# Performance work log

Hardware: AMD Instinct MI355X
Metric: run time of the kernel (lower is better)

## Reference

```python
import math
import jax, jax.numpy as jnp
import numpy as np

D_MODEL = 128
NUM_HEADS = 8
FACTOR = 5


def setup_inputs() -> dict:
    key = jax.random.key(0)
    ks = jax.random.split(key, 9)
    B, L, dm = 2, 4096, D_MODEL
    s = 1.0 / math.sqrt(dm)
    return {
        "x": jax.random.normal(ks[0], (B, L, dm), dtype=jnp.float32),
        "Wq": jax.random.normal(ks[1], (dm, dm), dtype=jnp.float32) * s,
        "bq": jnp.zeros((dm,), jnp.float32),
        "Wk": jax.random.normal(ks[2], (dm, dm), dtype=jnp.float32) * s,
        "bk": jnp.zeros((dm,), jnp.float32),
        "Wv": jax.random.normal(ks[3], (dm, dm), dtype=jnp.float32) * s,
        "bv": jnp.zeros((dm,), jnp.float32),
        "Wo": jax.random.normal(ks[4], (dm, dm), dtype=jnp.float32) * s,
        "bo": jnp.zeros((dm,), jnp.float32),
    }


def reference(x, Wq, bq, Wk, bk, Wv, bv, Wo, bo):
    B, L, dm = x.shape
    H = NUM_HEADS
    D = dm // H
    inv_sqrt_d = 1.0 / math.sqrt(D)

    def split_heads(t):  # [B,L,dm] -> [B,H,L,D]
        return t.reshape(B, L, H, D).transpose(0, 2, 1, 3)

    Q = split_heads(x @ Wq + bq)
    K = split_heads(x @ Wk + bk)
    V = split_heads(x @ Wv + bv)

    # sample_k = min(L_K, int(log(L_K) * factor)); L is static under jit
    sample_k = min(L, int(math.log(L) * FACTOR))

    # _prob_QK: full scores, per-query stable exp, mean over queries, top-k keys
    scores_full = jnp.einsum("bhqd,bhkd->bhqk", Q, K) * inv_sqrt_d  # [B,H,L,L]
    m = jnp.max(scores_full, axis=-1, keepdims=True)
    e = jnp.exp(scores_full - m)
    mean_attn = jnp.mean(e, axis=2)  # [B,H,L_K]
    _, idx = jax.lax.top_k(mean_attn, sample_k)  # [B,H,sample_k]

    # gather sampled keys/values along the key axis
    Ks = jnp.take_along_axis(K, idx[..., None], axis=2)  # [B,H,s,D]
    Vs = jnp.take_along_axis(V, idx[..., None], axis=2)

    attn = jax.nn.softmax(jnp.einsum("bhqd,bhsd->bhqs", Q, Ks) * inv_sqrt_d, axis=-1)
    out = jnp.einsum("bhqs,bhsd->bhqd", attn, Vs)  # [B,H,L,D]
    out = out.transpose(0, 2, 1, 3).reshape(B, L, dm)
    return out @ Wo + bo
```

## Files before the change

kernel.cpp:

```cpp
#include <hip/hip_runtime.h>
#include <hip/hip_bf16.h>

#define L 4096
#define DM 128
#define NH 8
#define HD 16
#define NBH 16
#define SK 41
#define NSPLIT 8
#define SLICE (L/NSPLIT)
#define NST (SLICE/32)
#define QSCALE 0.36067376022224085f

typedef __attribute__((ext_vector_type(8))) short s16x8;
typedef __attribute__((ext_vector_type(4))) float f32x4;
typedef __attribute__((ext_vector_type(16))) float f32x16;

__device__ __forceinline__ float bf2f(unsigned short h){ return __uint_as_float(((unsigned)h)<<16); }
__device__ __forceinline__ unsigned short f2bf(float f){
  unsigned u = __float_as_uint(f);
  u += 0x7FFFu + ((u>>16)&1u);
  return (unsigned short)(u>>16);
}
__device__ __forceinline__ float fast_exp2(float x){
  float r;
  asm("v_exp_f32 %0, %1" : "=v"(r) : "v"(x));
  return r;
}

__global__ __launch_bounds__(256) void prep(
    const float* __restrict__ x,
    const float* __restrict__ Wq, const float* __restrict__ Wk,
    const float* __restrict__ Wv, const float* __restrict__ Wo,
    unsigned short* __restrict__ Xh, unsigned short* __restrict__ Xl,
    unsigned short* __restrict__ Wph, unsigned short* __restrict__ Wpl)
{
  const int t = threadIdx.x;
  const int blk = blockIdx.x;
  if (blk < 1024){
    const long base = (long)blk*1024 + t*4;
    float4 v = *(const float4*)(x + base);
    unsigned short h[4], lo[4];
    h[0]=f2bf(v.x); lo[0]=f2bf(v.x - bf2f(h[0]));
    h[1]=f2bf(v.y); lo[1]=f2bf(v.y - bf2f(h[1]));
    h[2]=f2bf(v.z); lo[2]=f2bf(v.z - bf2f(h[2]));
    h[3]=f2bf(v.w); lo[3]=f2bf(v.w - bf2f(h[3]));
    *(uint2*)(Xh+base) = *(uint2*)h;
    *(uint2*)(Xl+base) = *(uint2*)lo;
  } else {
    const int e = (blk-1024)*256 + t;
    const int p = e >> 14;
    const int idx = e & 16383;
    const int j = idx & 7;
    const int f = idx >> 3;
    const int n = f & 127;
    const int kcg = f >> 7;
    const int k = (kcg>>1)*16 + (kcg&1)*8 + j;
    const float* W = (p==0)?Wq:((p==1)?Wk:((p==2)?Wv:Wo));
    const float v = W[k*128 + n];
    const unsigned short h = f2bf(v);
    Wph[e] = h;
    Wpl[e] = f2bf(v - bf2f(h));
  }
}

__global__ __launch_bounds__(256) void proj_mfma(
    const unsigned short* __restrict__ Xh, const unsigned short* __restrict__ Xl,
    const unsigned short* __restrict__ Wph, const unsigned short* __restrict__ Wpl,
    const float* __restrict__ bq, const float* __restrict__ bk, const float* __restrict__ bv,
    unsigned short* __restrict__ Qh, unsigned short* __restrict__ Ql,
    unsigned short* __restrict__ Kh, unsigned short* __restrict__ Kl,
    float* __restrict__ Vo)
{
  const int p = blockIdx.y;
  const float* __restrict__ bias = (p==0)?bq:((p==1)?bk:bv);
  __shared__ __align__(16) unsigned short wh[16384];
  __shared__ __align__(16) unsigned short wl[16384];
  const int t = threadIdx.x;
  {
    const uint4* gh = (const uint4*)(Wph + (long)p*16384);
    const uint4* gl = (const uint4*)(Wpl + (long)p*16384);
    uint4* sh = (uint4*)wh; uint4* sl = (uint4*)wl;
#pragma unroll
    for (int i=0;i<8;++i){ sh[t + i*256] = gh[t + i*256]; sl[t + i*256] = gl[t + i*256]; }
  }
  __syncthreads();
  const int w = t>>6, l = t&63;
  const int lc = l&15, g = l>>4;
  const int mbase = blockIdx.x*128 + w*32;
  f32x4 acc[2][8];
#pragma unroll
  for (int mt=0;mt<2;++mt)
#pragma unroll
    for (int nt=0;nt<8;++nt){ acc[mt][nt][0]=0.f; acc[mt][nt][1]=0.f; acc[mt][nt][2]=0.f; acc[mt][nt][3]=0.f; }
  const unsigned short* __restrict__ Asrc = (g<2)? Xh : Xl;
  const int koff = (g&1)*8;
  for (int kc=0; kc<8; ++kc){
    s16x8 a[2];
#pragma unroll
    for (int mt=0;mt<2;++mt)
      a[mt] = *(const s16x8*)(Asrc + ((long)(mbase + mt*16 + lc))*128 + kc*16 + koff);
#pragma unroll
    for (int nt=0;nt<8;++nt){
      const int fi = (kc*2+(g&1))*128 + nt*16 + lc;
      s16x8 b1 = ((const s16x8*)wh)[fi];
      s16x8 b2 = ((const s16x8*)wl)[fi];
#pragma unroll
      for (int mt=0;mt<2;++mt){
        acc[mt][nt] = __builtin_amdgcn_mfma_f32_16x16x32_bf16(a[mt], b1, acc[mt][nt], 0,0,0);
        acc[mt][nt] = __builtin_amdgcn_mfma_f32_16x16x32_bf16(a[mt], b2, acc[mt][nt], 0,0,0);
      }
    }
  }
#pragma unroll
  for (int nt=0;nt<8;++nt){
    const float bb = bias[nt*16 + lc];
#pragma unroll
    for (int mt=0;mt<2;++mt){
#pragma unroll
      for (int r=0;r<4;++r){
        const int row = mbase + mt*16 + g*4 + r;
        float v = acc[mt][nt][r] + bb;
        const int b = row>>12, li = row&4095;
        const long o = (((long)(b*NH + nt))*L + li)*HD + lc;
        if (p==2){
          Vo[o] = v;
        } else {
          if (p==0) v *= QSCALE;
          const unsigned short h = f2bf(v);
          const unsigned short lo2 = f2bf(v - bf2f(h));
          if (p==0){ Qh[o]=h; Ql[o]=lo2; } else { Kh[o]=h; Kl[o]=lo2; }
        }
      }
    }
  }
}

__global__ __launch_bounds__(256) void rowmax_k(
    const unsigned short* __restrict__ Qh, const unsigned short* __restrict__ Ql,
    const unsigned short* __restrict__ Kh, const unsigned short* __restrict__ Kl,
    float* __restrict__ mpart)
{
  const int bh = blockIdx.y, qt = blockIdx.x, ks = blockIdx.z;
  const int t = threadIdx.x, w = t>>6, l = t&63;
  const int lk = l&31, ks8 = (l>>5)*8;
  const int qbase = qt*256 + w*64;
  s16x8 ah0, al0, ah1, al1;
  {
    const long r0 = ((long)bh*L + qbase + lk)*HD + ks8;
    ah0 = *(const s16x8*)(Qh + r0);
    al0 = *(const s16x8*)(Ql + r0);
    ah1 = *(const s16x8*)(Qh + r0 + 32*HD);
    al1 = *(const s16x8*)(Ql + r0 + 32*HD);
  }
  f32x16 fz, rmax0, rmax1;
#pragma unroll
  for (int r=0;r<16;++r){ fz[r]=0.f; rmax0[r]=-3.4e38f; rmax1[r]=-3.4e38f; }
  const unsigned short* khp = Kh + ((long)bh*L + ks*SLICE + lk)*HD + ks8;
  const unsigned short* klp = Kl + ((long)bh*L + ks*SLICE + lk)*HD + ks8;
#pragma unroll 2
  for (int st=0; st<NST; ++st){
    s16x8 bhi = *(const s16x8*)(khp + st*32*HD);
    s16x8 blo = *(const s16x8*)(klp + st*32*HD);
    f32x16 a0 = __builtin_amdgcn_mfma_f32_32x32x16_bf16(ah0, bhi, fz, 0,0,0);
    a0 = __builtin_amdgcn_mfma_f32_32x32x16_bf16(al0, bhi, a0, 0,0,0);
    a0 = __builtin_amdgcn_mfma_f32_32x32x16_bf16(ah0, blo, a0, 0,0,0);
    f32x16 a1 = __builtin_amdgcn_mfma_f32_32x32x16_bf16(ah1, bhi, fz, 0,0,0);
    a1 = __builtin_amdgcn_mfma_f32_32x32x16_bf16(al1, bhi, a1, 0,0,0);
    a1 = __builtin_amdgcn_mfma_f32_32x32x16_bf16(ah1, blo, a1, 0,0,0);
#pragma unroll
    for (int r=0;r<16;++r){
      rmax0[r] = fmaxf(rmax0[r], a0[r]);
      rmax1[r] = fmaxf(rmax1[r], a1[r]);
    }
  }
  const long obase = ((long)ks*NBH + bh)*L + qbase + 4*(l>>5);
#pragma unroll
  for (int r=0;r<16;++r){
    float v0 = rmax0[r], v1 = rmax1[r];
    v0 = fmaxf(v0, __shfl_xor(v0,1));  v1 = fmaxf(v1, __shfl_xor(v1,1));
    v0 = fmaxf(v0, __shfl_xor(v0,2));  v1 = fmaxf(v1, __shfl_xor(v1,2));
    v0 = fmaxf(v0, __shfl_xor(v0,4));  v1 = fmaxf(v1, __shfl_xor(v1,4));
    v0 = fmaxf(v0, __shfl_xor(v0,8));  v1 = fmaxf(v1, __shfl_xor(v1,8));
    v0 = fmaxf(v0, __shfl_xor(v0,16)); v1 = fmaxf(v1, __shfl_xor(v1,16));
    if (lk == 0){
      const int rmap = (r&3) + 8*(r>>2);
      mpart[obase + rmap]      = v0;
      mpart[obase + 32 + rmap] = v1;
    }
  }
}

__global__ __launch_bounds__(256) void mreduce(
    const float* __restrict__ mpart, float* __restrict__ wq)
{
  const int i = blockIdx.x*256 + threadIdx.x;
  float m = -3.4e38f;
#pragma unroll
  for (int p=0;p<NSPLIT;++p) m = fmaxf(m, mpart[(long)p*NBH*L + i]);
  wq[i] = fast_exp2(-m);
}

__global__ __launch_bounds__(256) void colexp_k(
    const unsigned short* __restrict__ Kh, const unsigned short* __restrict__ Kl,
    const unsigned short* __restrict__ Qh, const unsigned short* __restrict__ Ql,
    const float* __restrict__ wq, float* __restrict__ cspart)
{
  const int bh = blockIdx.y, kt = blockIdx.x, qs = blockIdx.z;
  const int t = threadIdx.x, w = t>>6, l = t&63;
  const int lk = l&31, ks8 = (l>>5)*8;
  const int kbase = kt*256 + w*64;
  s16x8 ah0, al0, ah1, al1;
  {
    const long r0 = ((long)bh*L + kbase + lk)*HD + ks8;
    ah0 = *(const s16x8*)(Kh + r0);
    al0 = *(const s16x8*)(Kl + r0);
    ah1 = *(const s16x8*)(Kh + r0 + 32*HD);
    al1 = *(const s16x8*)(Kl + r0 + 32*HD);
  }
  f32x16 fz, cs0, cs1;
#pragma unroll
  for (int r=0;r<16;++r){ fz[r]=0.f; cs0[r]=0.f; cs1[r]=0.f; }
  const unsigned short* qhp = Qh + ((long)bh*L + qs*SLICE + lk)*HD + ks8;
  const unsigned short* qlp = Ql + ((long)bh*L + qs*SLICE + lk)*HD + ks8;
  const float* wgp = wq + (long)bh*L + qs*SLICE + lk;
#pragma unroll 2
  for (int st=0; st<NST; ++st){
    s16x8 bhi = *(const s16x8*)(qhp + st*32*HD);
    s16x8 blo = *(const s16x8*)(qlp + st*32*HD);
    const float wv = wgp[st*32];
    f32x16 a0 = __builtin_amdgcn_mfma_f32_32x32x16_bf16(ah0, bhi, fz, 0,0,0);
    a0 = __builtin_amdgcn_mfma_f32_32x32x16_bf16(al0, bhi, a0, 0,0,0);
    a0 = __builtin_amdgcn_mfma_f32_32x32x16_bf16(ah0, blo, a0, 0,0,0);
    f32x16 a1 = __builtin_amdgcn_mfma_f32_32x32x16_bf16(ah1, bhi, fz, 0,0,0);
    a1 = __builtin_amdgcn_mfma_f32_32x32x16_bf16(al1, bhi, a1, 0,0,0);
    a1 = __builtin_amdgcn_mfma_f32_32x32x16_bf16(ah1, blo, a1, 0,0,0);
#pragma unroll
    for (int r=0;r<16;++r){
      cs0[r] = fmaf(fast_exp2(a0[r]), wv, cs0[r]);
      cs1[r] = fmaf(fast_exp2(a1[r]), wv, cs1[r]);
    }
  }
  const long obase = ((long)qs*NBH + bh)*L + kbase + 4*(l>>5);
#pragma unroll
  for (int r=0;r<16;++r){
    float v0 = cs0[r], v1 = cs1[r];
    v0 += __shfl_xor(v0,1);  v1 += __shfl_xor(v1,1);
    v0 += __shfl_xor(v0,2);  v1 += __shfl_xor(v1,2);
    v0 += __shfl_xor(v0,4);  v1 += __shfl_xor(v1,4);
    v0 += __shfl_xor(v0,8);  v1 += __shfl_xor(v1,8);
    v0 += __shfl_xor(v0,16); v1 += __shfl_xor(v1,16);
    if (lk == 0){
      const int rmap = (r&3) + 8*(r>>2);
      cspart[obase + rmap]      = v0;
      cspart[obase + 32 + rmap] = v1;
    }
  }
}

__global__ __launch_bounds__(256) void topk_gather(
    const float* __restrict__ cspart,
    const unsigned short* __restrict__ Kh, const unsigned short* __restrict__ Kl,
    const float* __restrict__ V,
    float* __restrict__ Ks, float* __restrict__ Vs)
{
  const int bh = blockIdx.x;
  const int t = threadIdx.x;
  __shared__ float vals[4096];
  __shared__ unsigned hist[2048];
  __shared__ unsigned suf[256];
  __shared__ int meta[4];
  __shared__ int sel[SK];
  __shared__ int sorted[SK];
  __shared__ int tiei[4096];

  for (int i=t; i<1024; i+=256){
    float4 s = {0.f,0.f,0.f,0.f};
#pragma unroll
    for (int p=0;p<NSPLIT;++p){
      float4 v = *(const float4*)(cspart + ((long)p*NBH + bh)*L + i*4);
      s.x += v.x; s.y += v.y; s.z += v.z; s.w += v.w;
    }
    *(float4*)&vals[i*4] = s;
  }
  __syncthreads();

  int target = SK;
  unsigned B1 = 0, P2 = 0, T = 0;
#pragma unroll
  for (int pass=0; pass<3; ++pass){
    const int nb = (pass<2) ? 2048 : 1024;
    const int chunk = nb >> 8;
    for (int i=t;i<nb;i+=256) hist[i]=0u;
    __syncthreads();
    for (int i=t;i<4096;i+=256){
      const unsigned u = __float_as_uint(vals[i]);
      bool ok; int bk;
      if (pass==0){ ok = true;              bk = (int)(u>>21); }
      else if (pass==1){ ok = ((u>>21)==B1); bk = (int)((u>>10)&0x7FFu); }
      else { ok = ((u>>10)==P2);            bk = (int)(u&0x3FFu); }
      if (ok) atomicAdd(&hist[bk], 1u);
    }
    __syncthreads();
    {
      unsigned c=0;
#pragma unroll
      for (int b=0;b<8;++b) if (b<chunk) c += hist[t*chunk+b];
      suf[t]=c;
    }
    __syncthreads();
    for (int off=1; off<256; off<<=1){
      unsigned add = (t+off<256)? suf[t+off] : 0u;
      __syncthreads();
      suf[t] += add;
      __syncthreads();
    }
    {
      const unsigned mysuf = suf[t];
      const unsigned nxt = (t==255)?0u:suf[t+1];
      if (mysuf >= (unsigned)target && nxt < (unsigned)target){
        unsigned running = nxt;
        for (int b=t*chunk+chunk-1; b>=t*chunk; --b){
          const unsigned h = hist[b];
          if (running + h >= (unsigned)target){ meta[0]=b; meta[1]=(int)running; break; }
          running += h;
        }
      }
    }
    __syncthreads();
    const unsigned B = (unsigned)meta[0];
    target -= meta[1];
    if (pass==0) B1 = B;
    else if (pass==1) P2 = (B1<<11)|B;
    else T = (P2<<10)|B;
    __syncthreads();
  }
  if (t==0){ meta[2]=0; meta[3]=0; }
  __syncthreads();
  for (int i=t;i<4096;i+=256){
    const unsigned u = __float_as_uint(vals[i]);
    if (u > T){ int p = atomicAdd(&meta[2],1); sel[p]=i; }
    else if (u == T){ int p = atomicAdd(&meta[3],1); tiei[p]=i; }
  }
  __syncthreads();
  const int ngt = meta[2];
  const int ntie = meta[3];
  for (int j=t; j<ntie; j+=256){
    const int x = tiei[j];
    int rk=0;
    for (int k=0;k<ntie;++k) rk += (tiei[k] < x);
    if (rk < target) sel[ngt+rk] = x;
  }
  __syncthreads();
  if (t<SK){
    int x=sel[t]; int rk=0;
    for (int j=0;j<SK;++j) rk += (sel[j]<x);
    sorted[rk]=x;
  }
  __syncthreads();
  for (int i=t;i<SK*HD;i+=256){
    const int j=i>>4, dd=i&15;
    const int key=sorted[j];
    const long src=((long)bh*L+key)*HD+dd;
    Ks[(long)bh*SK*HD+i]=bf2f(Kh[src])+bf2f(Kl[src]);
    Vs[(long)bh*SK*HD+i]=V[src];
  }
}

__global__ __launch_bounds__(256) void sattn(
    const unsigned short* __restrict__ Qh, const unsigned short* __restrict__ Ql,
    const float* __restrict__ Ks, const float* __restrict__ Vs,
    unsigned short* __restrict__ AOh, unsigned short* __restrict__ AOl)
{
  const int bh = blockIdx.y, qb = blockIdx.x;
  const int t = threadIdx.x;
  __shared__ float ks[SK*HD], vs[SK*HD];
  for (int i=t; i<SK*HD; i+=256){
    ks[i] = Ks[(long)bh*SK*HD + i];
    vs[i] = Vs[(long)bh*SK*HD + i];
  }
  __syncthreads();
  const int q = qb*128 + (t>>1);
  const int half = t&1;
  const long qo = ((long)bh*L + q)*HD;
  float qv[16];
  {
    s16x8 h0 = *(const s16x8*)(Qh+qo);
    s16x8 h1 = *(const s16x8*)(Qh+qo+8);
    s16x8 l0 = *(const s16x8*)(Ql+qo);
    s16x8 l1 = *(const s16x8*)(Ql+qo+8);
#pragma unroll
    for (int d=0; d<8; ++d){
      qv[d]   = bf2f((unsigned short)h0[d]) + bf2f((unsigned short)l0[d]);
      qv[d+8] = bf2f((unsigned short)h1[d]) + bf2f((unsigned short)l1[d]);
    }
  }
  float mrun = -3.4e38f, lrun = 0.f, out[16];
#pragma unroll
  for (int d=0; d<16; ++d) out[d] = 0.f;
  for (int j=half; j<SK; j+=2){
    float4 k0 = *(const float4*)&ks[j*HD+0];
    float4 k1 = *(const float4*)&ks[j*HD+4];
    float4 k2 = *(const float4*)&ks[j*HD+8];
    float4 k3 = *(const float4*)&ks[j*HD+12];
    float s = qv[0]*k0.x;
    s = fmaf(qv[1],k0.y,s); s = fmaf(qv[2],k0.z,s); s = fmaf(qv[3],k0.w,s);
    s = fmaf(qv[4],k1.x,s); s = fmaf(qv[5],k1.y,s); s = fmaf(qv[6],k1.z,s); s = fmaf(qv[7],k1.w,s);
    s = fmaf(qv[8],k2.x,s); s = fmaf(qv[9],k2.y,s); s = fmaf(qv[10],k2.z,s); s = fmaf(qv[11],k2.w,s);
    s = fmaf(qv[12],k3.x,s); s = fmaf(qv[13],k3.y,s); s = fmaf(qv[14],k3.z,s); s = fmaf(qv[15],k3.w,s);
    if (s > mrun){
      const float c = fast_exp2(mrun - s);
      lrun *= c;
#pragma unroll
      for (int d=0; d<16; ++d) out[d] *= c;
      mrun = s;
    }
    const float p = fast_exp2(s - mrun);
    lrun += p;
    float4 v0 = *(const float4*)&vs[j*HD+0];
    float4 v1 = *(const float4*)&vs[j*HD+4];
    float4 v2 = *(const float4*)&vs[j*HD+8];
    float4 v3 = *(const float4*)&vs[j*HD+12];
    out[0]=fmaf(p,v0.x,out[0]); out[1]=fmaf(p,v0.y,out[1]); out[2]=fmaf(p,v0.z,out[2]); out[3]=fmaf(p,v0.w,out[3]);
    out[4]=fmaf(p,v1.x,out[4]); out[5]=fmaf(p,v1.y,out[5]); out[6]=fmaf(p,v1.z,out[6]); out[7]=fmaf(p,v1.w,out[7]);
    out[8]=fmaf(p,v2.x,out[8]); out[9]=fmaf(p,v2.y,out[9]); out[10]=fmaf(p,v2.z,out[10]); out[11]=fmaf(p,v2.w,out[11]);
    out[12]=fmaf(p,v3.x,out[12]); out[13]=fmaf(p,v3.y,out[13]); out[14]=fmaf(p,v3.z,out[14]); out[15]=fmaf(p,v3.w,out[15]);
  }
  const float mo = __shfl_xor(mrun, 1);
  const float lo = __shfl_xor(lrun, 1);
  const float mm = fmaxf(mrun, mo);
  const float cs_ = fast_exp2(mrun - mm);
  const float co_ = fast_exp2(mo - mm);
  const float ltot = fmaf(lrun, cs_, lo*co_);
  const float inv = 1.f / ltot;
#pragma unroll
  for (int d=0; d<16; ++d){
    const float ov = __shfl_xor(out[d], 1);
    out[d] = fmaf(out[d]*cs_, inv, ov*co_*inv);
  }
  if (half == 0){
    const int b = bh>>3, h = bh&7;
    const long row = (long)b*L + q;
    unsigned short hv[16], lv[16];
#pragma unroll
    for (int d=0; d<16; ++d){
      const float v = out[d];
      hv[d] = f2bf(v);
      lv[d] = f2bf(v - bf2f(hv[d]));
    }
    unsigned short* oh = AOh + row*DM + h*HD;
    unsigned short* ol = AOl + row*DM + h*HD;
    *(uint4*)(oh)   = *(uint4*)(hv);
    *(uint4*)(oh+8) = *(uint4*)(hv+8);
    *(uint4*)(ol)   = *(uint4*)(lv);
    *(uint4*)(ol+8) = *(uint4*)(lv+8);
  }
}

__global__ __launch_bounds__(256) void outproj_mfma(
    const unsigned short* __restrict__ AOh, const unsigned short* __restrict__ AOl,
    const unsigned short* __restrict__ Wph, const unsigned short* __restrict__ Wpl,
    const float* __restrict__ bo, float* __restrict__ out)
{
  __shared__ __align__(16) unsigned short wh[16384];
  __shared__ __align__(16) unsigned short wl[16384];
  const int t = threadIdx.x;
  {
    const uint4* gh = (const uint4*)(Wph + (long)3*16384);
    const uint4* gl = (const uint4*)(Wpl + (long)3*16384);
    uint4* sh = (uint4*)wh; uint4* sl = (uint4*)wl;
#pragma unroll
    for (int i=0;i<8;++i){ sh[t + i*256] = gh[t + i*256]; sl[t + i*256] = gl[t + i*256]; }
  }
  __syncthreads();
  const int w = t>>6, l = t&63;
  const int lc = l&15, g = l>>4;
  const int mbase = blockIdx.x*128 + w*32;
  f32x4 acc[2][8];
#pragma unroll
  for (int mt=0;mt<2;++mt)
#pragma unroll
    for (int nt=0;nt<8;++nt){ acc[mt][nt][0]=0.f; acc[mt][nt][1]=0.f; acc[mt][nt][2]=0.f; acc[mt][nt][3]=0.f; }
  const unsigned short* __restrict__ Asrc = (g<2)? AOh : AOl;
  const int koff = (g&1)*8;
  for (int kc=0; kc<8; ++kc){
    s16x8 a[2];
#pragma unroll
    for (int mt=0;mt<2;++mt)
      a[mt] = *(const s16x8*)(Asrc + ((long)(mbase + mt*16 + lc))*128 + kc*16 + koff);
#pragma unroll
    for (int nt=0;nt<8;++nt){
      const int fi = (kc*2+(g&1))*128 + nt*16 + lc;
      s16x8 b1 = ((const s16x8*)wh)[fi];
      s16x8 b2 = ((const s16x8*)wl)[fi];
#pragma unroll
      for (int mt=0;mt<2;++mt){
        acc[mt][nt] = __builtin_amdgcn_mfma_f32_16x16x32_bf16(a[mt], b1, acc[mt][nt], 0,0,0);
        acc[mt][nt] = __builtin_amdgcn_mfma_f32_16x16x32_bf16(a[mt], b2, acc[mt][nt], 0,0,0);
      }
    }
  }
#pragma unroll
  for (int nt=0;nt<8;++nt){
    const float bb = bo[nt*16 + lc];
#pragma unroll
    for (int mt=0;mt<2;++mt){
#pragma unroll
      for (int r=0;r<4;++r){
        const int row = mbase + mt*16 + g*4 + r;
        out[(long)row*DM + nt*16 + lc] = acc[mt][nt][r] + bb;
      }
    }
  }
}

extern "C" void kernel_launch(void* const* d_in, const int* in_sizes, int n_in,
                              void* d_out, int out_size, void* d_ws, size_t ws_size,
                              hipStream_t stream)
{
  const float* x  = (const float*)d_in[0];
  const float* Wq = (const float*)d_in[1];
  const float* bq = (const float*)d_in[2];
  const float* Wk = (const float*)d_in[3];
  const float* bk = (const float*)d_in[4];
  const float* Wv = (const float*)d_in[5];
  const float* bv = (const float*)d_in[6];
  const float* Wo = (const float*)d_in[7];
  const float* bo = (const float*)d_in[8];
  float* out = (float*)d_out;

  char* wsp = (char*)d_ws;
  size_t o = 0;
  auto alloc = [&](size_t bytes)->char*{
    char* p = wsp + o; o += (bytes + 255) & ~(size_t)255; return p;
  };
  unsigned short* Qh = (unsigned short*)alloc((size_t)NBH*L*HD*2);
  unsigned short* Ql = (unsigned short*)alloc((size_t)NBH*L*HD*2);
  unsigned short* Kh = (unsigned short*)alloc((size_t)NBH*L*HD*2);
  unsigned short* Kl = (unsigned short*)alloc((size_t)NBH*L*HD*2);
  float* Vv    = (float*)alloc((size_t)NBH*L*HD*4);
  float* mpart = (float*)alloc((size_t)NSPLIT*NBH*L*4);
  float* cspart= (float*)alloc((size_t)NSPLIT*NBH*L*4);
  float* wqv   = (float*)alloc((size_t)NBH*L*4);
  float* Ks    = (float*)alloc((size_t)NBH*SK*HD*4);
  float* Vs    = (float*)alloc((size_t)NBH*SK*HD*4);
  unsigned short* Xh  = (unsigned short*)alloc((size_t)2*L*DM*2);
  unsigned short* Xl  = (unsigned short*)alloc((size_t)2*L*DM*2);
  unsigned short* AOh = (unsigned short*)alloc((size_t)2*L*DM*2);
  unsigned short* AOl = (unsigned short*)alloc((size_t)2*L*DM*2);
  unsigned short* Wph = (unsigned short*)alloc((size_t)4*16384*2);
  unsigned short* Wpl = (unsigned short*)alloc((size_t)4*16384*2);

  prep<<<1280,256,0,stream>>>(x,Wq,Wk,Wv,Wo,Xh,Xl,Wph,Wpl);
  proj_mfma<<<dim3(64,3),256,0,stream>>>(Xh,Xl,Wph,Wpl,bq,bk,bv,Qh,Ql,Kh,Kl,Vv);
  rowmax_k<<<dim3(16,16,NSPLIT),256,0,stream>>>(Qh,Ql,Kh,Kl,mpart);
  mreduce<<<NBH*L/256,256,0,stream>>>(mpart,wqv);
  colexp_k<<<dim3(16,16,NSPLIT),256,0,stream>>>(Kh,Kl,Qh,Ql,wqv,cspart);
  topk_gather<<<16,256,0,stream>>>(cspart,Kh,Kl,Vv,Ks,Vs);
  sattn<<<dim3(32,16),256,0,stream>>>(Qh,Ql,Ks,Vs,AOh,AOl);
  outproj_mfma<<<64,256,0,stream>>>(AOh,AOl,Wph,Wpl,bo,out);
}
```

Measured before the change: 147.8 us.

## Widen rowmax and colexp wave tiles to 128 rows with register-prefetched operands

```diff
diff --git a/kernel.cpp b/kernel.cpp
--- a/kernel.cpp
+++ b/kernel.cpp
@@ -15,6 +15,8 @@
 typedef __attribute__((ext_vector_type(8))) short s16x8;
 typedef __attribute__((ext_vector_type(4))) float f32x4;
 typedef __attribute__((ext_vector_type(16))) float f32x16;
+
+#define MFMA32(A,B,C) __builtin_amdgcn_mfma_f32_32x32x16_bf16(A,B,C,0,0,0)
 
 __device__ __forceinline__ float bf2f(unsigned short h){ return __uint_as_float(((unsigned)h)<<16); }
 __device__ __forceinline__ unsigned short f2bf(float f){
@@ -144,49 +146,50 @@
   const int bh = blockIdx.y, qt = blockIdx.x, ks = blockIdx.z;
   const int t = threadIdx.x, w = t>>6, l = t&63;
   const int lk = l&31, ks8 = (l>>5)*8;
-  const int qbase = qt*256 + w*64;
-  s16x8 ah0, al0, ah1, al1;
+  const int qbase = qt*512 + w*128;
+  s16x8 ah0,ah1,ah2,ah3, al0,al1,al2,al3;
   {
     const long r0 = ((long)bh*L + qbase + lk)*HD + ks8;
-    ah0 = *(const s16x8*)(Qh + r0);
-    al0 = *(const s16x8*)(Ql + r0);
-    ah1 = *(const s16x8*)(Qh + r0 + 32*HD);
-    al1 = *(const s16x8*)(Ql + r0 + 32*HD);
-  }
-  f32x16 fz, rmax0, rmax1;
-#pragma unroll
-  for (int r=0;r<16;++r){ fz[r]=0.f; rmax0[r]=-3.4e38f; rmax1[r]=-3.4e38f; }
+    ah0 = *(const s16x8*)(Qh + r0);          al0 = *(const s16x8*)(Ql + r0);
+    ah1 = *(const s16x8*)(Qh + r0 + 32*HD);  al1 = *(const s16x8*)(Ql + r0 + 32*HD);
+    ah2 = *(const s16x8*)(Qh + r0 + 64*HD);  al2 = *(const s16x8*)(Ql + r0 + 64*HD);
+    ah3 = *(const s16x8*)(Qh + r0 + 96*HD);  al3 = *(const s16x8*)(Ql + r0 + 96*HD);
+  }
+  f32x16 fz, m0, m1, m2, m3;
+#pragma unroll
+  for (int r=0;r<16;++r){ fz[r]=0.f; m0[r]=-3.4e38f; m1[r]=-3.4e38f; m2[r]=-3.4e38f; m3[r]=-3.4e38f; }
   const unsigned short* khp = Kh + ((long)bh*L + ks*SLICE + lk)*HD + ks8;
   const unsigned short* klp = Kl + ((long)bh*L + ks*SLICE + lk)*HD + ks8;
-#pragma unroll 2
+  s16x8 cb1 = *(const s16x8*)khp;
+  s16x8 cb2 = *(const s16x8*)klp;
   for (int st=0; st<NST; ++st){
-    s16x8 bhi = *(const s16x8*)(khp + st*32*HD);
-    s16x8 blo = *(const s16x8*)(klp + st*32*HD);
-    f32x16 a0 = __builtin_amdgcn_mfma_f32_32x32x16_bf16(ah0, bhi, fz, 0,0,0);
-    a0 = __builtin_amdgcn_mfma_f32_32x32x16_bf16(al0, bhi, a0, 0,0,0);
-    a0 = __builtin_amdgcn_mfma_f32_32x32x16_bf16(ah0, blo, a0, 0,0,0);
-    f32x16 a1 = __builtin_amdgcn_mfma_f32_32x32x16_bf16(ah1, bhi, fz, 0,0,0);
-    a1 = __builtin_amdgcn_mfma_f32_32x32x16_bf16(al1, bhi, a1, 0,0,0);
-    a1 = __builtin_amdgcn_mfma_f32_32x32x16_bf16(ah1, blo, a1, 0,0,0);
-#pragma unroll
-    for (int r=0;r<16;++r){
-      rmax0[r] = fmaxf(rmax0[r], a0[r]);
-      rmax1[r] = fmaxf(rmax1[r], a1[r]);
-    }
+    s16x8 nb1 = *(const s16x8*)(khp + (st+1)*32*HD);
+    s16x8 nb2 = *(const s16x8*)(klp + (st+1)*32*HD);
+    f32x16 x0 = MFMA32(ah0,cb1,fz); x0 = MFMA32(al0,cb1,x0); x0 = MFMA32(ah0,cb2,x0);
+    f32x16 x1 = MFMA32(ah1,cb1,fz); x1 = MFMA32(al1,cb1,x1); x1 = MFMA32(ah1,cb2,x1);
+#pragma unroll
+    for (int r=0;r<16;++r){ m0[r] = fmaxf(m0[r], x0[r]); m1[r] = fmaxf(m1[r], x1[r]); }
+    f32x16 x2 = MFMA32(ah2,cb1,fz); x2 = MFMA32(al2,cb1,x2); x2 = MFMA32(ah2,cb2,x2);
+    f32x16 x3 = MFMA32(ah3,cb1,fz); x3 = MFMA32(al3,cb1,x3); x3 = MFMA32(ah3,cb2,x3);
+#pragma unroll
+    for (int r=0;r<16;++r){ m2[r] = fmaxf(m2[r], x2[r]); m3[r] = fmaxf(m3[r], x3[r]); }
+    cb1 = nb1; cb2 = nb2;
   }
   const long obase = ((long)ks*NBH + bh)*L + qbase + 4*(l>>5);
 #pragma unroll
   for (int r=0;r<16;++r){
-    float v0 = rmax0[r], v1 = rmax1[r];
-    v0 = fmaxf(v0, __shfl_xor(v0,1));  v1 = fmaxf(v1, __shfl_xor(v1,1));
-    v0 = fmaxf(v0, __shfl_xor(v0,2));  v1 = fmaxf(v1, __shfl_xor(v1,2));
-    v0 = fmaxf(v0, __shfl_xor(v0,4));  v1 = fmaxf(v1, __shfl_xor(v1,4));
-    v0 = fmaxf(v0, __shfl_xor(v0,8));  v1 = fmaxf(v1, __shfl_xor(v1,8));
-    v0 = fmaxf(v0, __shfl_xor(v0,16)); v1 = fmaxf(v1, __shfl_xor(v1,16));
+    float v0=m0[r], v1=m1[r], v2=m2[r], v3=m3[r];
+    v0=fmaxf(v0,__shfl_xor(v0,1));  v1=fmaxf(v1,__shfl_xor(v1,1));  v2=fmaxf(v2,__shfl_xor(v2,1));  v3=fmaxf(v3,__shfl_xor(v3,1));
+    v0=fmaxf(v0,__shfl_xor(v0,2));  v1=fmaxf(v1,__shfl_xor(v1,2));  v2=fmaxf(v2,__shfl_xor(v2,2));  v3=fmaxf(v3,__shfl_xor(v3,2));
+    v0=fmaxf(v0,__shfl_xor(v0,4));  v1=fmaxf(v1,__shfl_xor(v1,4));  v2=fmaxf(v2,__shfl_xor(v2,4));  v3=fmaxf(v3,__shfl_xor(v3,4));
+    v0=fmaxf(v0,__shfl_xor(v0,8));  v1=fmaxf(v1,__shfl_xor(v1,8));  v2=fmaxf(v2,__shfl_xor(v2,8));  v3=fmaxf(v3,__shfl_xor(v3,8));
+    v0=fmaxf(v0,__shfl_xor(v0,16)); v1=fmaxf(v1,__shfl_xor(v1,16)); v2=fmaxf(v2,__shfl_xor(v2,16)); v3=fmaxf(v3,__shfl_xor(v3,16));
     if (lk == 0){
       const int rmap = (r&3) + 8*(r>>2);
       mpart[obase + rmap]      = v0;
       mpart[obase + 32 + rmap] = v1;
+      mpart[obase + 64 + rmap] = v2;
+      mpart[obase + 96 + rmap] = v3;
     }
   }
 }
@@ -209,51 +212,59 @@
   const int bh = blockIdx.y, kt = blockIdx.x, qs = blockIdx.z;
   const int t = threadIdx.x, w = t>>6, l = t&63;
   const int lk = l&31, ks8 = (l>>5)*8;
-  const int kbase = kt*256 + w*64;
-  s16x8 ah0, al0, ah1, al1;
+  const int kbase = kt*512 + w*128;
+  s16x8 ah0,ah1,ah2,ah3, al0,al1,al2,al3;
   {
     const long r0 = ((long)bh*L + kbase + lk)*HD + ks8;
-    ah0 = *(const s16x8*)(Kh + r0);
-    al0 = *(const s16x8*)(Kl + r0);
-    ah1 = *(const s16x8*)(Kh + r0 + 32*HD);
-    al1 = *(const s16x8*)(Kl + r0 + 32*HD);
-  }
-  f32x16 fz, cs0, cs1;
-#pragma unroll
-  for (int r=0;r<16;++r){ fz[r]=0.f; cs0[r]=0.f; cs1[r]=0.f; }
+    ah0 = *(const s16x8*)(Kh + r0);          al0 = *(const s16x8*)(Kl + r0);
+    ah1 = *(const s16x8*)(Kh + r0 + 32*HD);  al1 = *(const s16x8*)(Kl + r0 + 32*HD);
+    ah2 = *(const s16x8*)(Kh + r0 + 64*HD);  al2 = *(const s16x8*)(Kl + r0 + 64*HD);
+    ah3 = *(const s16x8*)(Kh + r0 + 96*HD);  al3 = *(const s16x8*)(Kl + r0 + 96*HD);
+  }
+  f32x16 fz, cs0, cs1, cs2, cs3;
+#pragma unroll
+  for (int r=0;r<16;++r){ fz[r]=0.f; cs0[r]=0.f; cs1[r]=0.f; cs2[r]=0.f; cs3[r]=0.f; }
   const unsigned short* qhp = Qh + ((long)bh*L + qs*SLICE + lk)*HD + ks8;
   const unsigned short* qlp = Ql + ((long)bh*L + qs*SLICE + lk)*HD + ks8;
   const float* wgp = wq + (long)bh*L + qs*SLICE + lk;
-#pragma unroll 2
+  s16x8 cb1 = *(const s16x8*)qhp;
+  s16x8 cb2 = *(const s16x8*)qlp;
+  float cw = wgp[0];
   for (int st=0; st<NST; ++st){
-    s16x8 bhi = *(const s16x8*)(qhp + st*32*HD);
-    s16x8 blo = *(const s16x8*)(qlp + st*32*HD);
-    const float wv = wgp[st*32];
-    f32x16 a0 = __builtin_amdgcn_mfma_f32_32x32x16_bf16(ah0, bhi, fz, 0,0,0);
-    a0 = __builtin_amdgcn_mfma_f32_32x32x16_bf16(al0, bhi, a0, 0,0,0);
-    a0 = __builtin_amdgcn_mfma_f32_32x32x16_bf16(ah0, blo, a0, 0,0,0);
-    f32x16 a1 = __builtin_amdgcn_mfma_f32_32x32x16_bf16(ah1, bhi, fz, 0,0,0);
-    a1 = __builtin_amdgcn_mfma_f32_32x32x16_bf16(al1, bhi, a1, 0,0,0);
-    a1 = __builtin_amdgcn_mfma_f32_32x32x16_bf16(ah1, blo, a1, 0,0,0);
+    s16x8 nb1 = *(const s16x8*)(qhp + (st+1)*32*HD);
+    s16x8 nb2 = *(const s16x8*)(qlp + (st+1)*32*HD);
+    const float nw = wgp[(st+1)*32];
+    f32x16 x0 = MFMA32(ah0,cb1,fz); x0 = MFMA32(al0,cb1,x0); x0 = MFMA32(ah0,cb2,x0);
+    f32x16 x1 = MFMA32(ah1,cb1,fz); x1 = MFMA32(al1,cb1,x1); x1 = MFMA32(ah1,cb2,x1);
 #pragma unroll
     for (int r=0;r<16;++r){
-      cs0[r] = fmaf(fast_exp2(a0[r]), wv, cs0[r]);
-      cs1[r] = fmaf(fast_exp2(a1[r]), wv, cs1[r]);
-    }
+      cs0[r] = fmaf(fast_exp2(x0[r]), cw, cs0[r]);
+      cs1[r] = fmaf(fast_exp2(x1[r]), cw, cs1[r]);
+    }
+    f32x16 x2 = MFMA32(ah2,cb1,fz); x2 = MFMA32(al2,cb1,x2); x2 = MFMA32(ah2,cb2,x2);
+    f32x16 x3 = MFMA32(ah3,cb1,fz); x3 = MFMA32(al3,cb1,x3); x3 = MFMA32(ah3,cb2,x3);
+#pragma unroll
+    for (int r=0;r<16;++r){
+      cs2[r] = fmaf(fast_exp2(x2[r]), cw, cs2[r]);
+      cs3[r] = fmaf(fast_exp2(x3[r]), cw, cs3[r]);
+    }
+    cb1 = nb1; cb2 = nb2; cw = nw;
   }
   const long obase = ((long)qs*NBH + bh)*L + kbase + 4*(l>>5);
 #pragma unroll
   for (int r=0;r<16;++r){
-    float v0 = cs0[r], v1 = cs1[r];
-    v0 += __shfl_xor(v0,1);  v1 += __shfl_xor(v1,1);
-    v0 += __shfl_xor(v0,2);  v1 += __shfl_xor(v1,2);
-    v0 += __shfl_xor(v0,4);  v1 += __shfl_xor(v1,4);
-    v0 += __shfl_xor(v0,8);  v1 += __shfl_xor(v1,8);
-    v0 += __shfl_xor(v0,16); v1 += __shfl_xor(v1,16);
+    float v0=cs0[r], v1=cs1[r], v2=cs2[r], v3=cs3[r];
+    v0+=__shfl_xor(v0,1);  v1+=__shfl_xor(v1,1);  v2+=__shfl_xor(v2,1);  v3+=__shfl_xor(v3,1);
+    v0+=__shfl_xor(v0,2);  v1+=__shfl_xor(v1,2);  v2+=__shfl_xor(v2,2);  v3+=__shfl_xor(v3,2);
+    v0+=__shfl_xor(v0,4);  v1+=__shfl_xor(v1,4);  v2+=__shfl_xor(v2,4);  v3+=__shfl_xor(v3,4);
+    v0+=__shfl_xor(v0,8);  v1+=__shfl_xor(v1,8);  v2+=__shfl_xor(v2,8);  v3+=__shfl_xor(v3,8);
+    v0+=__shfl_xor(v0,16); v1+=__shfl_xor(v1,16); v2+=__shfl_xor(v2,16); v3+=__shfl_xor(v3,16);
     if (lk == 0){
       const int rmap = (r&3) + 8*(r>>2);
       cspart[obase + rmap]      = v0;
       cspart[obase + 32 + rmap] = v1;
+      cspart[obase + 64 + rmap] = v2;
+      cspart[obase + 96 + rmap] = v3;
     }
   }
 }
@@ -553,9 +564,9 @@
 
   prep<<<1280,256,0,stream>>>(x,Wq,Wk,Wv,Wo,Xh,Xl,Wph,Wpl);
   proj_mfma<<<dim3(64,3),256,0,stream>>>(Xh,Xl,Wph,Wpl,bq,bk,bv,Qh,Ql,Kh,Kl,Vv);
-  rowmax_k<<<dim3(16,16,NSPLIT),256,0,stream>>>(Qh,Ql,Kh,Kl,mpart);
+  rowmax_k<<<dim3(8,16,NSPLIT),256,0,stream>>>(Qh,Ql,Kh,Kl,mpart);
   mreduce<<<NBH*L/256,256,0,stream>>>(mpart,wqv);
-  colexp_k<<<dim3(16,16,NSPLIT),256,0,stream>>>(Kh,Kl,Qh,Ql,wqv,cspart);
+  colexp_k<<<dim3(8,16,NSPLIT),256,0,stream>>>(Kh,Kl,Qh,Ql,wqv,cspart);
   topk_gather<<<16,256,0,stream>>>(cspart,Kh,Kl,Vv,Ks,Vs);
   sattn<<<dim3(32,16),256,0,stream>>>(Qh,Ql,Ks,Vs,AOh,AOl);
   outproj_mfma<<<64,256,0,stream>>>(AOh,AOl,Wph,Wpl,bo,out);
```

New measurement: 153.5 us. +3.9%, slower.
